# Kernel optimization log

Hardware: AMD Instinct MI355X
Metric: run time of the kernel (lower is better)

Reference implementation:

```python
import jax, jax.numpy as jnp
import numpy as np

N_STEPS = 96
BATCH = 16384
N_MAT = 8
N_STRIKES = 8
PERIOD = 12          # N_steps // n_maturities
T_HORIZON = 1.0
RFR = 0.03
S0 = 1.0
LAYER = 128
DT = T_HORIZON / N_STEPS
SQRT_DT = float(np.sqrt(DT))
DF = float(np.exp(-RFR * DT))  # per-step discount factor


def _mlp(Win, bin_, Wh, bh, Wout, bout, x, out_fn):
    # x: [features, batch]; linear layers act on axis 0 (matches torch cat along dim 0)
    h = jax.nn.leaky_relu(Win @ x + bin_[:, None])
    for k in range(Wh.shape[0]):
        h = jax.nn.leaky_relu(Wh[k] @ h + bh[k][:, None])
    return out_fn(Wout @ h + bout[:, None])


def _forward(normals, strikes, lev_Win, lev_bin, lev_Wh, lev_bh, lev_Wout, lev_bout,
             hed_Win, hed_bin, hed_Wh, hed_bh, hed_Wout, hed_bout):
    B = normals.shape[1]
    dt = jnp.float32(DT)
    sqrt_dt = jnp.float32(SQRT_DT)
    r = jnp.float32(RFR)
    df = jnp.float32(DF)
    sg = jax.lax.stop_gradient

    def body(carry, xs):
        S_prev, hedging, prices, variance = carry
        i, nn_i = xs                      # i: int32 step (1..N_STEPS), nn_i: [B] normals
        i_f = i.astype(jnp.float32)
        idx = (i - 1) // PERIOD           # which per-period MLP
        t = ((i_f - 1.0) * dt) * jnp.ones((1, B), jnp.float32)
        X = jnp.concatenate([t, S_prev], axis=0)          # [2, B]
        lev = _mlp(lev_Win[idx], lev_bin[idx], lev_Wh[idx], lev_bh[idx],
                   lev_Wout[idx], lev_bout[idx], X, jax.nn.softplus)  # [1, B]
        drift = S_prev * r / (1.0 + jnp.abs(sg(S_prev) * r) * sqrt_dt)
        diffusion = S_prev * lev / (1.0 + jnp.abs(sg(S_prev * lev)) * sqrt_dt)
        dW = sqrt_dt * nn_i                               # [B]
        S_curr = S_prev + drift * dt + diffusion * dW     # [1, B]
        Xh = jnp.concatenate([t, sg(S_prev)], axis=0)
        hedge = _mlp(hed_Win[idx], hed_bin[idx], hed_Wh[idx], hed_bh[idx],
                     hed_Wout[idx], hed_bout[idx], Xh,
                     lambda y: y).reshape(N_STRIKES, N_MAT, B)
        hedging = hedging + (df ** (i_f - 1.0)) * sg(S_prev * diffusion) * hedge * dW
        # maturity handling (maturities at steps PERIOD, 2*PERIOD, ..., N_STEPS)
        table_idx = jnp.clip(i // PERIOD - 1, 0, N_MAT - 1)
        is_mat = (i % PERIOD == 0).astype(jnp.float32)
        simulated = (df ** i_f) * jnp.maximum(S_curr - strikes[:, None], 0.0) \
                    - hedging[:, table_idx]               # [K, B]
        mean = simulated.mean(axis=1)                     # [K]
        var = jnp.sum((simulated - mean[:, None]) ** 2, axis=1) / (B - 1)  # unbiased, as torch .var()
        prices = prices.at[:, table_idx].add(is_mat * mean)
        variance = variance.at[:, table_idx].add(is_mat * var)
        return (S_curr, hedging, prices, variance), None

    body = jax.checkpoint(body)
    carry0 = (jnp.full((1, B), jnp.float32(S0)),
              jnp.zeros((N_STRIKES, N_MAT, B), jnp.float32),
              jnp.zeros((N_STRIKES, N_MAT), jnp.float32),
              jnp.zeros((N_STRIKES, N_MAT), jnp.float32))
    xs = (jnp.arange(1, N_STEPS + 1, dtype=jnp.int32), normals)
    (_, _, prices, variance), _ = jax.lax.scan(body, carry0, xs)
    return prices, variance


def setup_inputs() -> dict:
    key = jax.random.key(0)
    ks = jax.random.split(key, 16)
    M, L, NH = N_MAT, LAYER, 3  # num_layers=4 -> 3 hidden-to-hidden layers

    def w(k, shape, fan_in):
        return (jax.random.normal(k, shape, jnp.float32) / np.sqrt(fan_in)).astype(jnp.float32)

    inp = {
        "normals": jax.random.normal(ks[0], (N_STEPS, BATCH), jnp.float32),
        "strikes": jnp.linspace(0.8, 1.15, N_STRIKES, dtype=jnp.float32),
        "lev_Win": w(ks[1], (M, L, 2), 2),
        "lev_bin": w(ks[2], (M, L), L),
        "lev_Wh": w(ks[3], (M, NH, L, L), L),
        "lev_bh": w(ks[4], (M, NH, L), L),
        "lev_Wout": w(ks[5], (M, 1, L), L),
        "lev_bout": w(ks[6], (M, 1), L),
        "hed_Win": w(ks[7], (M, L, 2), 2),
        "hed_bin": w(ks[8], (M, L), L),
        "hed_Wh": w(ks[9], (M, NH, L, L), L),
        "hed_bh": w(ks[10], (M, NH, L), L),
        "hed_Wout": w(ks[11], (M, N_STRIKES * N_MAT, L), L),
        "hed_bout": w(ks[12], (M, N_STRIKES * N_MAT), L),
    }
    return inp


def reference(normals, strikes, lev_Win, lev_bin, lev_Wh, lev_bh, lev_Wout, lev_bout,
              hed_Win, hed_bin, hed_Wh, hed_bh, hed_Wout, hed_bout):
    return _forward(normals, strikes, lev_Win, lev_bin, lev_Wh, lev_bh, lev_Wout, lev_bout,
                    hed_Win, hed_bin, hed_Wh, hed_bh, hed_Wout, hed_bout)
```

## Files before the change

kernel.cpp:

```cpp
#include <hip/hip_runtime.h>
#include <math.h>

typedef __attribute__((ext_vector_type(8)))  short  short8;
typedef __attribute__((ext_vector_type(4)))  short  short4v;
typedef __attribute__((ext_vector_type(16))) float  f32x16;
typedef __attribute__((ext_vector_type(4)))  float  f32x4v;

#define DT_F    ((float)(1.0/96.0))
#define SQDT_F  (0.10206207261596575f)
#define DF_F    (0.99968754882437816f)
#define RFR_F   (0.03f)

#define LDS_L1  32768
#define LDS_H1  49152
#define LDS_SS  65536
#define LDS_HC  66048

static __device__ __forceinline__ short f2bf(float x) {
    return __builtin_bit_cast(short, (__bf16)x);
}
static __device__ __forceinline__ float bf2f(short h) {
    return (float)__builtin_bit_cast(__bf16, h);
}
static __device__ __forceinline__ short8 ldsr16(const char* p) {
    return *(const short8*)__builtin_assume_aligned(p, 16);
}
static __device__ __forceinline__ void ldsw8(char* p, short4v v) {
    *(short4v*)__builtin_assume_aligned(p, 8) = v;
}

__device__ __forceinline__ void layer1(const float* __restrict__ Win, const float* __restrict__ bin_,
        float t, const float* __restrict__ sScur, char* __restrict__ lds, int wl1, int wvm, int l)
{
    const int g = l >> 4, c15 = l & 15;
    const int r0 = (wvm << 5) + (g << 3);
    float a8[8], w1[8];
#pragma unroll
    for (int jj = 0; jj < 8; ++jj) {
        const int r = r0 + jj;
        a8[jj] = fmaf(Win[2*r], t, bin_[r]);
        w1[jj] = Win[2*r + 1];
    }
#pragma unroll
    for (int cc = 0; cc < 4; ++cc) {
        const float S = sScur[c15 + (cc << 4)];
        short8 v;
#pragma unroll
        for (int jj = 0; jj < 8; ++jj) {
            float h = fmaf(w1[jj], S, a8[jj]);
            h = fmaxf(h, 0.01f * h);
            v[jj] = f2bf(h);
        }
        *(short8*)__builtin_assume_aligned(lds + wl1 + (cc << 12), 16) = v;
    }
}

__device__ __forceinline__ void hidden32(char* __restrict__ lds,
        const int (&__restrict__ rdk)[8], const int (&__restrict__ wrq)[4],
        int rdImm, int wrImm,
        const ushort* __restrict__ WFm, const float* __restrict__ bias,
        int wvm, int l, int l5)
{
    f32x16 a0e, a1e;
    f32x16 a0o = {0,0,0,0,0,0,0,0,0,0,0,0,0,0,0,0};
    f32x16 a1o = a0o;
#pragma unroll
    for (int q = 0; q < 4; ++q) {
        const f32x4v bq = *(const f32x4v*)&bias[(wvm << 5) + (q << 3) + (l5 << 2)];
#pragma unroll
        for (int ii = 0; ii < 4; ++ii) {
            a0e[(q << 2) + ii] = bq[ii];
            a1e[(q << 2) + ii] = bq[ii];
        }
    }
    const short8* fb = (const short8*)(WFm + (wvm << 12));
#pragma unroll
    for (int kc = 0; kc < 8; kc += 2) {
        short8 aE = fb[kc * 64 + l];
        short8 aO = fb[(kc + 1) * 64 + l];
        short8 b0e = ldsr16(lds + rdk[kc]     + rdImm);
        short8 b1e = ldsr16(lds + rdk[kc]     + rdImm + 8192);
        short8 b0o = ldsr16(lds + rdk[kc + 1] + rdImm);
        short8 b1o = ldsr16(lds + rdk[kc + 1] + rdImm + 8192);
        a0e = __builtin_amdgcn_mfma_f32_32x32x16_bf16(aE, b0e, a0e, 0, 0, 0);
        a1e = __builtin_amdgcn_mfma_f32_32x32x16_bf16(aE, b1e, a1e, 0, 0, 0);
        a0o = __builtin_amdgcn_mfma_f32_32x32x16_bf16(aO, b0o, a0o, 0, 0, 0);
        a1o = __builtin_amdgcn_mfma_f32_32x32x16_bf16(aO, b1o, a1o, 0, 0, 0);
    }
    const f32x16 acc0 = a0e + a0o;
    const f32x16 acc1 = a1e + a1o;
#pragma unroll
    for (int q = 0; q < 4; ++q) {
        short4v o0, o1;
#pragma unroll
        for (int ii = 0; ii < 4; ++ii) {
            float x0 = acc0[(q << 2) + ii]; o0[ii] = f2bf(fmaxf(x0, 0.01f * x0));
            float x1 = acc1[(q << 2) + ii]; o1[ii] = f2bf(fmaxf(x1, 0.01f * x1));
        }
        ldsw8(lds + wrq[q] + wrImm,        o0);
        ldsw8(lds + wrq[q] + wrImm + 8192, o1);
    }
}

__global__ __launch_bounds__(512, 2)
void sim_kernel(const float* __restrict__ normals, const float* __restrict__ strikes,
                const float* __restrict__ levWin, const float* __restrict__ levbin,
                const float* __restrict__ levbh,  const float* __restrict__ levWout,
                const float* __restrict__ levbout,
                const float* __restrict__ hedWin, const float* __restrict__ hedbin,
                const float* __restrict__ hedbh,  const float* __restrict__ hedbout,
                const ushort* __restrict__ WF, double* __restrict__ accD)
{
    __shared__ char lds[66560];
    float* sSb = (float*)(lds + LDS_SS);
    float* sHc = (float*)(lds + LDS_HC);

    const int tid  = threadIdx.x;
    const int wv   = tid >> 6;
    const int half = wv >> 2;
    const int wvm  = wv & 3;
    const int l    = tid & 63;
    const int g    = l >> 4;
    const int c15  = l & 15;
    const int c0   = l & 31;
    const int l5   = l >> 5;
    const int bp0  = blockIdx.x * 64;

    const int chainoff = half << 14;
    const int rbase = chainoff + (c0 << 8) + ((l5 ^ (c0 & 1)) << 4);
    const int pxor  = ((c0 >> 1) & 7) << 5;
    int rdk[8];
#pragma unroll
    for (int kc = 0; kc < 8; ++kc) rdk[kc] = rbase + ((kc << 5) ^ pxor);
    int wrq[4];
#pragma unroll
    for (int q = 0; q < 4; ++q)
        wrq[q] = chainoff + (c0 << 8) + (l5 << 3)
               + ((q ^ (c0 & 3)) << 4) + ((wvm ^ ((c0 >> 2) & 3)) << 6);
    const int wl1 = chainoff + (c15 << 8) + ((g ^ (c15 & 3)) << 4)
                  + ((wvm ^ ((c15 >> 2) & 3)) << 6);
    int rout[4];
    if (half == 0) {
        const int cl = c15 + (wvm << 4);
        const int ob = LDS_L1 + (cl << 8) + ((g ^ ((cl >> 2) & 3)) << 6);
#pragma unroll
        for (int kb = 0; kb < 4; ++kb) rout[kb] = ob + ((kb ^ (cl & 3)) << 4);
    } else {
        const int ob = LDS_H1 + (c15 << 8) + (((l >> 4) ^ (c15 & 3)) << 4);
        const int px2 = ((c15 >> 2) & 3) << 6;
#pragma unroll
        for (int kcq = 0; kcq < 4; ++kcq) rout[kcq] = ob + ((kcq << 6) ^ px2);
    }

    if (tid < 64) sSb[tid] = 1.0f;
    float hedg[4][4];
#pragma unroll
    for (int a = 0; a < 4; ++a)
#pragma unroll
        for (int b = 0; b < 4; ++b) hedg[a][b] = 0.f;
    float dfim1 = 1.0f;
    __syncthreads();

    for (int i = 1; i <= 96; ++i) {
        const int idx = (i - 1) / 12;
        const float t = (float)(i - 1) * DT_F;
        const float* sScur = sSb + (((i - 1) & 1) << 6);
        float* sSnxt = sSb + ((i & 1) << 6);
        const ushort* WFi = WF + (size_t)idx * 106496;

        const float* Win  = (half ? hedWin : levWin) + idx * 256;
        const float* binp = (half ? hedbin : levbin) + (idx << 7);
        const float* bh   = (half ? hedbh  : levbh)  + idx * 384;
        const ushort* Wm  = WFi + ((half * 3) << 14);

        layer1(Win, binp, t, sScur, lds, wl1, wvm, l);
        float nrm = 0.f;
        if (half == 0) nrm = normals[(size_t)(i - 1) * 16384 + bp0 + c15 + (wvm << 4)];
        __syncthreads();
        hidden32(lds, rdk, wrq, 0,     32768, Wm,         bh,       wvm, l, l5);
        __syncthreads();
        hidden32(lds, rdk, wrq, 32768, 0,     Wm + 16384, bh + 128, wvm, l, l5);
        __syncthreads();
        hidden32(lds, rdk, wrq, 0,     32768, Wm + 32768, bh + 256, wvm, l, l5);
        __syncthreads();

        const float dfi = dfim1 * DF_F;
        f32x4v acc0 = {0,0,0,0}, acc1 = acc0, acc2 = acc0, acc3 = acc0;
        if (half == 0) {
            const float* Wo = levWout + (idx << 7);
            float wk[32];
#pragma unroll
            for (int kb = 0; kb < 8; ++kb)
                *(f32x4v*)&wk[4 * kb] = *(const f32x4v*)&Wo[(g << 5) + (kb << 2)];
            const int c = c15 + (wvm << 4);
            float p = 0.f;
#pragma unroll
            for (int kb = 0; kb < 4; ++kb) {
                short8 hv = ldsr16(lds + rout[kb]);
#pragma unroll
                for (int j = 0; j < 8; ++j) p = fmaf(bf2f(hv[j]), wk[(kb << 3) + j], p);
            }
            p += __shfl_xor(p, 16);
            p += __shfl_xor(p, 32);
            p += levbout[idx];
            const float lv = (p > 20.f) ? p : __logf(1.f + __expf(p));
            const float S = sScur[c];
            const float drift = S * RFR_F / (1.f + fabsf(S * RFR_F) * SQDT_F);
            const float dif   = S * lv    / (1.f + fabsf(S * lv)   * SQDT_F);
            const float dW = SQDT_F * nrm;
            const float Sn = S + drift * DT_F + dif * dW;
            if (g == 0) { sSnxt[c] = Sn; sHc[c] = dfim1 * (S * dif) * dW; }
        } else {
            const short8* fb = (const short8*)(WFi + 98304 + (wvm << 11));
            __builtin_amdgcn_s_setprio(1);
#pragma unroll
            for (int kcq = 0; kcq < 4; ++kcq) {
                short8 a = fb[kcq * 64 + l];
                short8 b0 = ldsr16(lds + rout[kcq]);
                short8 b1 = ldsr16(lds + rout[kcq] + 4096);
                short8 b2 = ldsr16(lds + rout[kcq] + 8192);
                short8 b3 = ldsr16(lds + rout[kcq] + 12288);
                acc0 = __builtin_amdgcn_mfma_f32_16x16x32_bf16(a, b0, acc0, 0, 0, 0);
                acc1 = __builtin_amdgcn_mfma_f32_16x16x32_bf16(a, b1, acc1, 0, 0, 0);
                acc2 = __builtin_amdgcn_mfma_f32_16x16x32_bf16(a, b2, acc2, 0, 0, 0);
                acc3 = __builtin_amdgcn_mfma_f32_16x16x32_bf16(a, b3, acc3, 0, 0, 0);
            }
            __builtin_amdgcn_s_setprio(0);
        }
        __syncthreads();

        if (half == 1) {
            const f32x4v bo4 = *(const f32x4v*)&hedbout[(idx << 6) + (wvm << 4) + (g << 2)];
            const float hc0 = sHc[c15], hc1 = sHc[16 + c15], hc2 = sHc[32 + c15], hc3 = sHc[48 + c15];
#pragma unroll
            for (int ii = 0; ii < 4; ++ii) {
                hedg[0][ii] = fmaf(hc0, acc0[ii] + bo4[ii], hedg[0][ii]);
                hedg[1][ii] = fmaf(hc1, acc1[ii] + bo4[ii], hedg[1][ii]);
                hedg[2][ii] = fmaf(hc2, acc2[ii] + bo4[ii], hedg[2][ii]);
                hedg[3][ii] = fmaf(hc3, acc3[ii] + bo4[ii], hedg[3][ii]);
            }
            if ((i % 12) == 0) {
                const int m = i / 12 - 1;
                const int isel = m & 3;
                const bool active = ((m >> 2) == (g & 1));
                const int ks = (wvm << 1) + (g >> 1);
                float s_ = 0.f, q_ = 0.f;
                if (active) {
                    const float K = strikes[ks];
#pragma unroll
                    for (int ct = 0; ct < 4; ++ct) {
                        const float* hrow = hedg[ct];
                        const float hv = (isel == 0) ? hrow[0] : (isel == 1) ? hrow[1]
                                        : (isel == 2) ? hrow[2] : hrow[3];
                        const float Sn = sSnxt[(ct << 4) + c15];
                        const float sim = dfi * fmaxf(Sn - K, 0.f) - hv;
                        s_ += sim; q_ += sim * sim;
                    }
                }
#pragma unroll
                for (int off = 1; off < 16; off <<= 1) {
                    s_ += __shfl_xor(s_, off);
                    q_ += __shfl_xor(q_, off);
                }
                if (active && c15 == 0) {
                    const int rep = blockIdx.x & 31;
                    atomicAdd(&accD[rep * 128 + ks * 8 + m], (double)s_);
                    atomicAdd(&accD[rep * 128 + 64 + ks * 8 + m], (double)q_);
                }
            }
        }
        dfim1 = dfi;
    }
}

__global__ void prep_kernel(const float* __restrict__ levWh, const float* __restrict__ hedWh,
                            const float* __restrict__ hedWout,
                            ushort* __restrict__ WF, double* __restrict__ accD)
{
    const long long stride = (long long)gridDim.x * blockDim.x;
    const long long t0 = (long long)blockIdx.x * blockDim.x + threadIdx.x;
    for (long long e = t0; e < 851968LL; e += stride) {
        const int idx = (int)(e / 106496);
        const int rem = (int)(e % 106496);
        float val;
        if (rem < 98304) {
            const int m    = rem >> 14;
            const int r2   = rem & 16383;
            const int slot = r2 >> 9;
            const int rb   = slot >> 3;
            const int kc   = slot & 7;
            const int lane = (r2 >> 3) & 63;
            const int j    = r2 & 7;
            const int r = (rb << 5) + (lane & 31);
            const int k = (kc << 4) + ((lane >> 5) << 3) + j;
            const float* src = (m < 3) ? levWh : hedWh;
            const int mm = (m < 3) ? m : m - 3;
            val = src[(((idx * 3 + mm) << 7) + r) * 128 + k];
        } else {
            const int r3   = rem - 98304;
            const int slot = r3 >> 9;
            const int rb   = slot >> 2;
            const int kcq  = slot & 3;
            const int lane = (r3 >> 3) & 63;
            const int j    = r3 & 7;
            const int r = (rb << 4) + (lane & 15);
            const int k = (kcq << 5) + ((lane >> 4) << 3) + j;
            val = hedWout[(idx << 13) + (r << 7) + k];
        }
        WF[e] = (ushort)f2bf(val);
    }
    for (long long e = t0; e < 4096; e += stride) accD[e] = 0.0;
}

__global__ void finalize_kernel(const double* __restrict__ accD, float* __restrict__ out)
{
    const int t = threadIdx.x;
    if (t < 64) {
        double s = 0.0, q = 0.0;
        for (int rep = 0; rep < 32; ++rep) {
            s += accD[rep * 128 + t];
            q += accD[rep * 128 + 64 + t];
        }
        out[t]      = (float)(s / 16384.0);
        out[64 + t] = (float)((q - s * s / 16384.0) / 16383.0);
    }
}

extern "C" void kernel_launch(void* const* d_in, const int* in_sizes, int n_in,
                              void* d_out, int out_size, void* d_ws, size_t ws_size,
                              hipStream_t stream)
{
    const float* normals = (const float*)d_in[0];
    const float* strikes = (const float*)d_in[1];
    const float* levWin  = (const float*)d_in[2];
    const float* levbin  = (const float*)d_in[3];
    const float* levWh   = (const float*)d_in[4];
    const float* levbh   = (const float*)d_in[5];
    const float* levWout = (const float*)d_in[6];
    const float* levbout = (const float*)d_in[7];
    const float* hedWin  = (const float*)d_in[8];
    const float* hedbin  = (const float*)d_in[9];
    const float* hedWh   = (const float*)d_in[10];
    const float* hedbh   = (const float*)d_in[11];
    const float* hedWout = (const float*)d_in[12];
    const float* hedbout = (const float*)d_in[13];

    ushort* WF   = (ushort*)d_ws;
    double* accD = (double*)((char*)d_ws + 1703936);

    prep_kernel<<<1024, 256, 0, stream>>>(levWh, hedWh, hedWout, WF, accD);
    sim_kernel<<<256, 512, 0, stream>>>(normals, strikes,
                                        levWin, levbin, levbh, levWout, levbout,
                                        hedWin, hedbin, hedbh, hedbout,
                                        WF, accD);
    finalize_kernel<<<1, 64, 0, stream>>>(accD, (float*)d_out);
}
```

Before: 564.9 us.

## Prefetch per-layer MFMA weights into registers and use lightweight LDS-only barriers

Each hidden layer's bf16 weight fragments are now loaded from global memory into registers one layer ahead (double-buffered wfA/wfB), so the global load latency overlaps the previous layer's MFMAs instead of stalling inside the MFMA loop. The output-layer weights and bias are also fetched before the last hidden layer, and the bias is folded into the accumulator init. __syncthreads is replaced by a barrier that waits only on lgkmcnt, so outstanding global loads need not drain at each barrier. This costs extra VGPRs (16 short8 plus 4) under a 512x2 launch bound, with risk of spills or lower occupancy, and it relies on every cross-wave dependency going through LDS.

```diff
diff --git a/kernel.cpp b/kernel.cpp
--- a/kernel.cpp
+++ b/kernel.cpp
@@ -29,6 +29,21 @@
     *(short4v*)__builtin_assume_aligned(p, 8) = v;
 }
 
+static __device__ __forceinline__ void soft_barrier() {
+    asm volatile("" ::: "memory");
+    asm volatile("s_waitcnt lgkmcnt(0)" ::: "memory");
+    __builtin_amdgcn_s_barrier();
+    asm volatile("" ::: "memory");
+}
+
+static __device__ __forceinline__ void prefA(const ushort* __restrict__ Wm,
+        int wvm, int l, short8 (&__restrict__ wf)[8])
+{
+    const short8* fb = (const short8*)(Wm + (wvm << 12));
+#pragma unroll
+    for (int kc = 0; kc < 8; ++kc) wf[kc] = fb[kc * 64 + l];
+}
+
 __device__ __forceinline__ void layer1(const float* __restrict__ Win, const float* __restrict__ bin_,
         float t, const float* __restrict__ sScur, char* __restrict__ lds, int wl1, int wvm, int l)
 {
@@ -58,7 +73,7 @@
 __device__ __forceinline__ void hidden32(char* __restrict__ lds,
         const int (&__restrict__ rdk)[8], const int (&__restrict__ wrq)[4],
         int rdImm, int wrImm,
-        const ushort* __restrict__ WFm, const float* __restrict__ bias,
+        const short8 (&__restrict__ wf)[8], const float* __restrict__ bias,
         int wvm, int l, int l5)
 {
     f32x16 a0e, a1e;
@@ -73,19 +88,16 @@
             a1e[(q << 2) + ii] = bq[ii];
         }
     }
-    const short8* fb = (const short8*)(WFm + (wvm << 12));
 #pragma unroll
     for (int kc = 0; kc < 8; kc += 2) {
-        short8 aE = fb[kc * 64 + l];
-        short8 aO = fb[(kc + 1) * 64 + l];
         short8 b0e = ldsr16(lds + rdk[kc]     + rdImm);
         short8 b1e = ldsr16(lds + rdk[kc]     + rdImm + 8192);
         short8 b0o = ldsr16(lds + rdk[kc + 1] + rdImm);
         short8 b1o = ldsr16(lds + rdk[kc + 1] + rdImm + 8192);
-        a0e = __builtin_amdgcn_mfma_f32_32x32x16_bf16(aE, b0e, a0e, 0, 0, 0);
-        a1e = __builtin_amdgcn_mfma_f32_32x32x16_bf16(aE, b1e, a1e, 0, 0, 0);
-        a0o = __builtin_amdgcn_mfma_f32_32x32x16_bf16(aO, b0o, a0o, 0, 0, 0);
-        a1o = __builtin_amdgcn_mfma_f32_32x32x16_bf16(aO, b1o, a1o, 0, 0, 0);
+        a0e = __builtin_amdgcn_mfma_f32_32x32x16_bf16(wf[kc],     b0e, a0e, 0, 0, 0);
+        a1e = __builtin_amdgcn_mfma_f32_32x32x16_bf16(wf[kc],     b1e, a1e, 0, 0, 0);
+        a0o = __builtin_amdgcn_mfma_f32_32x32x16_bf16(wf[kc + 1], b0o, a0o, 0, 0, 0);
+        a1o = __builtin_amdgcn_mfma_f32_32x32x16_bf16(wf[kc + 1], b1o, a1o, 0, 0, 0);
     }
     const f32x16 acc0 = a0e + a0o;
     const f32x16 acc1 = a1e + a1o;
@@ -159,6 +171,8 @@
 #pragma unroll
         for (int b = 0; b < 4; ++b) hedg[a][b] = 0.f;
     float dfim1 = 1.0f;
+
+    short8 wfA[8], wfB[8];
     __syncthreads();
 
     for (int i = 1; i <= 96; ++i) {
@@ -173,19 +187,33 @@
         const float* bh   = (half ? hedbh  : levbh)  + idx * 384;
         const ushort* Wm  = WFi + ((half * 3) << 14);
 
+        prefA(Wm, wvm, l, wfA);
         layer1(Win, binp, t, sScur, lds, wl1, wvm, l);
         float nrm = 0.f;
         if (half == 0) nrm = normals[(size_t)(i - 1) * 16384 + bp0 + c15 + (wvm << 4)];
-        __syncthreads();
-        hidden32(lds, rdk, wrq, 0,     32768, Wm,         bh,       wvm, l, l5);
-        __syncthreads();
-        hidden32(lds, rdk, wrq, 32768, 0,     Wm + 16384, bh + 128, wvm, l, l5);
-        __syncthreads();
-        hidden32(lds, rdk, wrq, 0,     32768, Wm + 32768, bh + 256, wvm, l, l5);
-        __syncthreads();
+        soft_barrier();
+
+        prefA(Wm + 16384, wvm, l, wfB);
+        hidden32(lds, rdk, wrq, 0,     32768, wfA, bh,       wvm, l, l5);
+        soft_barrier();
+
+        prefA(Wm + 32768, wvm, l, wfA);
+        hidden32(lds, rdk, wrq, 32768, 0,     wfB, bh + 128, wvm, l, l5);
+        soft_barrier();
+
+        short8 wOut[4];
+        f32x4v bo4;
+        if (half == 1) {
+            const short8* fo = (const short8*)(WFi + 98304 + (wvm << 11));
+#pragma unroll
+            for (int kcq = 0; kcq < 4; ++kcq) wOut[kcq] = fo[kcq * 64 + l];
+            bo4 = *(const f32x4v*)&hedbout[(idx << 6) + (wvm << 4) + (g << 2)];
+        }
+        hidden32(lds, rdk, wrq, 0,     32768, wfA, bh + 256, wvm, l, l5);
+        soft_barrier();
 
         const float dfi = dfim1 * DF_F;
-        f32x4v acc0 = {0,0,0,0}, acc1 = acc0, acc2 = acc0, acc3 = acc0;
+        f32x4v acc0, acc1, acc2, acc3;
         if (half == 0) {
             const float* Wo = levWout + (idx << 7);
             float wk[32];
@@ -211,33 +239,31 @@
             const float Sn = S + drift * DT_F + dif * dW;
             if (g == 0) { sSnxt[c] = Sn; sHc[c] = dfim1 * (S * dif) * dW; }
         } else {
-            const short8* fb = (const short8*)(WFi + 98304 + (wvm << 11));
+            acc0 = bo4; acc1 = bo4; acc2 = bo4; acc3 = bo4;
             __builtin_amdgcn_s_setprio(1);
 #pragma unroll
             for (int kcq = 0; kcq < 4; ++kcq) {
-                short8 a = fb[kcq * 64 + l];
                 short8 b0 = ldsr16(lds + rout[kcq]);
                 short8 b1 = ldsr16(lds + rout[kcq] + 4096);
                 short8 b2 = ldsr16(lds + rout[kcq] + 8192);
                 short8 b3 = ldsr16(lds + rout[kcq] + 12288);
-                acc0 = __builtin_amdgcn_mfma_f32_16x16x32_bf16(a, b0, acc0, 0, 0, 0);
-                acc1 = __builtin_amdgcn_mfma_f32_16x16x32_bf16(a, b1, acc1, 0, 0, 0);
-                acc2 = __builtin_amdgcn_mfma_f32_16x16x32_bf16(a, b2, acc2, 0, 0, 0);
-                acc3 = __builtin_amdgcn_mfma_f32_16x16x32_bf16(a, b3, acc3, 0, 0, 0);
+                acc0 = __builtin_amdgcn_mfma_f32_16x16x32_bf16(wOut[kcq], b0, acc0, 0, 0, 0);
+                acc1 = __builtin_amdgcn_mfma_f32_16x16x32_bf16(wOut[kcq], b1, acc1, 0, 0, 0);
+                acc2 = __builtin_amdgcn_mfma_f32_16x16x32_bf16(wOut[kcq], b2, acc2, 0, 0, 0);
+                acc3 = __builtin_amdgcn_mfma_f32_16x16x32_bf16(wOut[kcq], b3, acc3, 0, 0, 0);
             }
             __builtin_amdgcn_s_setprio(0);
         }
-        __syncthreads();
+        soft_barrier();
 
         if (half == 1) {
-            const f32x4v bo4 = *(const f32x4v*)&hedbout[(idx << 6) + (wvm << 4) + (g << 2)];
             const float hc0 = sHc[c15], hc1 = sHc[16 + c15], hc2 = sHc[32 + c15], hc3 = sHc[48 + c15];
 #pragma unroll
             for (int ii = 0; ii < 4; ++ii) {
-                hedg[0][ii] = fmaf(hc0, acc0[ii] + bo4[ii], hedg[0][ii]);
-                hedg[1][ii] = fmaf(hc1, acc1[ii] + bo4[ii], hedg[1][ii]);
-                hedg[2][ii] = fmaf(hc2, acc2[ii] + bo4[ii], hedg[2][ii]);
-                hedg[3][ii] = fmaf(hc3, acc3[ii] + bo4[ii], hedg[3][ii]);
+                hedg[0][ii] = fmaf(hc0, acc0[ii], hedg[0][ii]);
+                hedg[1][ii] = fmaf(hc1, acc1[ii], hedg[1][ii]);
+                hedg[2][ii] = fmaf(hc2, acc2[ii], hedg[2][ii]);
+                hedg[3][ii] = fmaf(hc3, acc3[ii], hedg[3][ii]);
             }
             if ((i % 12) == 0) {
                 const int m = i / 12 - 1;
```

Result: faster. 536.6 us, median of 2 (-5.0%).
